# Kernel optimization log

Hardware: AMD Instinct MI355X
Metric: run time of the kernel (lower is better)

The kernel has to match this reference:

```python
import jax, jax.numpy as jnp
import numpy as np

DVEC = 128
B, S = 4, 1024


def setup_inputs() -> dict:
    key = jax.random.key(0)
    k1, k2 = jax.random.split(key)
    func_and_arg = jax.random.normal(k1, (B, S, 2 * DVEC), dtype=jnp.float32)
    cooccurrences = jax.random.normal(k2, (DVEC, DVEC, DVEC), dtype=jnp.float32)
    return {"func_and_arg": func_and_arg, "cooccurrences": cooccurrences}


def reference(func_and_arg, cooccurrences):
    # out[b,s,z] = sum_{i,j} func[b,s,i] * cooc[i,j,z] * arg[b,s,j]
    d = cooccurrences.shape[0]
    func = func_and_arg[..., :d]   # [B,S,D]
    arg = func_and_arg[..., d:]    # [B,S,D]
    # contract func over i first -> [B,S,D(j),Z], then arg over j -> [B,S,Z]
    tmp = jnp.einsum('bsi,ijz->bsjz', func, cooccurrences)
    return jnp.einsum('bsjz,bsj->bsz', tmp, arg)
```

## Files before the change

### kernel.cpp

```cpp
#include <hip/hip_runtime.h>
#include <hip/hip_bf16.h>


typedef __attribute__((ext_vector_type(8))) short bf16x8;
typedef __attribute__((ext_vector_type(4))) float f32x4;

__device__ __forceinline__ unsigned pkbf16(float x, float y) {
    __hip_bfloat162 h = __float22bfloat162_rn(make_float2(x, y));
    unsigned u; __builtin_memcpy(&u, &h, sizeof(u));
    return u;
}
__device__ __forceinline__ float bf16lo(unsigned u) {
    unsigned v = u << 16; float f; __builtin_memcpy(&f, &v, 4); return f;
}
__device__ __forceinline__ float bf16hi(unsigned u) {
    unsigned v = u & 0xFFFF0000u; float f; __builtin_memcpy(&f, &v, 4); return f;
}

__global__ __launch_bounds__(256) void cooc_prep(
    const float* __restrict__ Cc, const float* __restrict__ fa,
    ushort* __restrict__ CT, ushort* __restrict__ APK)
{
    const int bid = blockIdx.x;
    const int t = threadIdx.x;
    if (bid < 512) {
        __shared__ float tile[32][132];
        const int i  = bid >> 2;
        const int j0 = (bid & 3) * 32;
        {
            const int jj = t >> 3;
            const int zb = (t & 7) * 16;
            const float* src = Cc + (size_t)i * 16384 + (size_t)(j0 + jj) * 128 + zb;
            #pragma unroll
            for (int k = 0; k < 4; ++k)
                *(float4*)&tile[jj][zb + k * 4] = *(const float4*)(src + k * 4);
        }
        __syncthreads();
        {
            const int z = t >> 1;
            const int h = t & 1;
            unsigned o[8];
            #pragma unroll
            for (int p = 0; p < 8; ++p)
                o[p] = pkbf16(tile[h * 16 + 2 * p][z], tile[h * 16 + 2 * p + 1][z]);
            const int c0 = (j0 >> 3) + h * 2;
            ushort* dst = CT + (size_t)i * 16384 + (size_t)(z >> 4) * 2048
                             + (size_t)c0 * 128 + (z & 15) * 8;
            *(uint4*)dst         = make_uint4(o[0], o[1], o[2], o[3]);
            *(uint4*)(dst + 128) = make_uint4(o[4], o[5], o[6], o[7]);
        }
    } else {
        const int g = bid - 512;
        const int ks = t >> 6, lk = (t >> 4) & 3, lm = t & 15;
        (void)ks; (void)lk; (void)lm;
        const float* src = fa + (size_t)(g * 16 + (t & 15)) * 256 + 128
                              + (t >> 6) * 32 + ((t >> 4) & 3) * 8;
        float4 q0 = *(const float4*)src;
        float4 q1 = *(const float4*)(src + 4);
        *(uint4*)(APK + (size_t)g * 2048 + t * 8) =
            make_uint4(pkbf16(q0.x, q0.y), pkbf16(q0.z, q0.w),
                       pkbf16(q1.x, q1.y), pkbf16(q1.z, q1.w));
    }
}

template<int USE_WS>
__global__ __launch_bounds__(256, 3) void cooc_main(
    const float* __restrict__ fa, const ushort* __restrict__ CT,
    const ushort* __restrict__ APK, float* __restrict__ dst)
{
    __shared__ ushort fpk[16][128];

    const int bid = blockIdx.x;
    const int kp = bid & 7, zp = (bid >> 3) & 3, mtile = bid >> 5;
    const int t0 = mtile * 128, i0 = kp * 16;
    const int tid = threadIdx.x, lane = tid & 63, wv = tid >> 6;
    const int mg = wv >> 1, zg = wv & 1;
    const int lm = lane & 15, lk = lane >> 4;

    {
        const int row = tid & 127;
        const int sh = (tid >> 7) * 8;
        const float* fp = fa + (size_t)(t0 + row) * 256 + i0 + sh;
        float4 v0 = *(const float4*)fp;
        float4 v1 = *(const float4*)(fp + 4);
        fpk[sh + 0][row] = (ushort)(pkbf16(v0.x, v0.x) & 0xFFFF);
        fpk[sh + 1][row] = (ushort)(pkbf16(v0.y, v0.y) & 0xFFFF);
        fpk[sh + 2][row] = (ushort)(pkbf16(v0.z, v0.z) & 0xFFFF);
        fpk[sh + 3][row] = (ushort)(pkbf16(v0.w, v0.w) & 0xFFFF);
        fpk[sh + 4][row] = (ushort)(pkbf16(v1.x, v1.x) & 0xFFFF);
        fpk[sh + 5][row] = (ushort)(pkbf16(v1.y, v1.y) & 0xFFFF);
        fpk[sh + 6][row] = (ushort)(pkbf16(v1.z, v1.z) & 0xFFFF);
        fpk[sh + 7][row] = (ushort)(pkbf16(v1.w, v1.w) & 0xFFFF);
    }

    bf16x8 a_pk[4][4];
    {
        const ushort* ap = APK + (size_t)((t0 >> 4) + mg * 4) * 2048 + lane * 8;
        #pragma unroll
        for (int m = 0; m < 4; ++m)
            #pragma unroll
            for (int ks = 0; ks < 4; ++ks)
                a_pk[m][ks] = *(const bf16x8*)(ap + (size_t)m * 2048 + ks * 512);
    }

    const ushort* bbase = CT + (size_t)i0 * 16384
                             + (size_t)(zp * 2 + zg) * 2048 + lane * 8;

    bf16x8 Bg[2][4];
    #pragma unroll
    for (int c = 0; c < 4; ++c)
        Bg[0][c] = *(const bf16x8*)(bbase + c * 512);

    __syncthreads();

    float acc[4][4];
    #pragma unroll
    for (int m = 0; m < 4; ++m)
        #pragma unroll
        for (int r = 0; r < 4; ++r) acc[m][r] = 0.f;

    #pragma unroll 2
    for (int s = 0; s < 16; ++s) {
        const int cur = s & 1;

        if (s < 15) {
            const ushort* p = bbase + (size_t)(s + 1) * 16384;
            #pragma unroll
            for (int c = 0; c < 4; ++c)
                Bg[cur ^ 1][c] = *(const bf16x8*)(p + c * 512);
        }

        uint2 fq[4];
        #pragma unroll
        for (int m = 0; m < 4; ++m)
            fq[m] = *(const uint2*)&fpk[s][mg * 64 + m * 16 + lk * 4];

        f32x4 g[4];
        #pragma unroll
        for (int m = 0; m < 4; ++m) g[m] = (f32x4){0.f, 0.f, 0.f, 0.f};
        #pragma unroll
        for (int ks = 0; ks < 4; ++ks)
            #pragma unroll
            for (int m = 0; m < 4; ++m)
                g[m] = __builtin_amdgcn_mfma_f32_16x16x32_bf16(
                    a_pk[m][ks], Bg[cur][ks], g[m], 0, 0, 0);

        #pragma unroll
        for (int m = 0; m < 4; ++m) {
            acc[m][0] += bf16lo(fq[m].x) * g[m][0];
            acc[m][1] += bf16hi(fq[m].x) * g[m][1];
            acc[m][2] += bf16lo(fq[m].y) * g[m][2];
            acc[m][3] += bf16hi(fq[m].y) * g[m][3];
        }
    }

    const int col = zp * 32 + zg * 16 + lm;
    #pragma unroll
    for (int m = 0; m < 4; ++m)
        #pragma unroll
        for (int r = 0; r < 4; ++r) {
            const int row = t0 + mg * 64 + m * 16 + lk * 4 + r;
            if (USE_WS)
                dst[(size_t)kp * 524288 + (size_t)row * 128 + col] = acc[m][r];
            else
                atomicAdd(&dst[(size_t)row * 128 + col], acc[m][r]);
        }
}

__global__ __launch_bounds__(256) void cooc_reduce(const float* __restrict__ ws,
                                                   float* __restrict__ out) {
    const size_t idx = ((size_t)blockIdx.x * 256 + threadIdx.x) * 4;
    float4 a = *(const float4*)(ws + idx);
    #pragma unroll
    for (int k = 1; k < 8; ++k) {
        float4 b = *(const float4*)(ws + (size_t)k * 524288 + idx);
        a.x += b.x; a.y += b.y; a.z += b.z; a.w += b.w;
    }
    *(float4*)(out + idx) = a;
}

extern "C" void kernel_launch(void* const* d_in, const int* in_sizes, int n_in,
                              void* d_out, int out_size, void* d_ws, size_t ws_size,
                              hipStream_t stream) {
    const float* fa = (const float*)d_in[0];
    const float* Cc = (const float*)d_in[1];
    float* out = (float*)d_out;

    const size_t PART = (size_t)8 * 524288;
    const size_t CTOF = PART * sizeof(float);
    const size_t CTSZ = (size_t)128 * 128 * 128 * 2;
    const size_t APOF = CTOF + CTSZ;
    const size_t APSZ = (size_t)4096 * 128 * 2;
    const size_t NEED_FULL = APOF + APSZ;
    const size_t NEED_CT   = CTSZ + APSZ;

    if (ws_size >= NEED_FULL) {
        ushort* CT  = (ushort*)((char*)d_ws + CTOF);
        ushort* APK = (ushort*)((char*)d_ws + APOF);
        cooc_prep<<<768, 256, 0, stream>>>(Cc, fa, CT, APK);
        cooc_main<1><<<1024, 256, 0, stream>>>(fa, CT, APK, (float*)d_ws);
        cooc_reduce<<<512, 256, 0, stream>>>((const float*)d_ws, out);
    } else if (ws_size >= NEED_CT) {
        ushort* CT  = (ushort*)d_ws;
        ushort* APK = (ushort*)((char*)d_ws + CTSZ);
        cooc_prep<<<768, 256, 0, stream>>>(Cc, fa, CT, APK);
        (void)hipMemsetAsync(out, 0, (size_t)out_size * sizeof(float), stream);
        cooc_main<0><<<1024, 256, 0, stream>>>(fa, CT, APK, out);
    } else {
        (void)hipMemsetAsync(out, 0, (size_t)out_size * sizeof(float), stream);
        cooc_main<0><<<1024, 256, 0, stream>>>(fa, (const ushort*)d_ws,
                                               (const ushort*)d_ws, out);
    }
}
```

Before: 85.48 us.

## Double z-columns per wave to reuse A fragments, keep func in fp32 LDS

Each wave now computes two 16-wide z tiles instead of one. The A fragments held in registers and the func values in shared memory are reused across both tiles, and the grid is halved from 1024 to 512 blocks. Func values are stored as fp32 in shared memory, which removes the bf16 pack/unpack and uses the unrounded scale. This raises register pressure, so the occupancy hint drops to 2 blocks per CU, and having fewer blocks may lower latency hiding.

Result: no change. 84.63 us (-1.0%).

```diff
diff --git a/kernel.cpp b/kernel.cpp
--- a/kernel.cpp
+++ b/kernel.cpp
@@ -9,12 +9,6 @@
     __hip_bfloat162 h = __float22bfloat162_rn(make_float2(x, y));
     unsigned u; __builtin_memcpy(&u, &h, sizeof(u));
     return u;
-}
-__device__ __forceinline__ float bf16lo(unsigned u) {
-    unsigned v = u << 16; float f; __builtin_memcpy(&f, &v, 4); return f;
-}
-__device__ __forceinline__ float bf16hi(unsigned u) {
-    unsigned v = u & 0xFFFF0000u; float f; __builtin_memcpy(&f, &v, 4); return f;
 }
 
 __global__ __launch_bounds__(256) void cooc_prep(
@@ -51,8 +45,6 @@
         }
     } else {
         const int g = bid - 512;
-        const int ks = t >> 6, lk = (t >> 4) & 3, lm = t & 15;
-        (void)ks; (void)lk; (void)lm;
         const float* src = fa + (size_t)(g * 16 + (t & 15)) * 256 + 128
                               + (t >> 6) * 32 + ((t >> 4) & 3) * 8;
         float4 q0 = *(const float4*)src;
@@ -64,14 +56,14 @@
 }
 
 template<int USE_WS>
-__global__ __launch_bounds__(256, 3) void cooc_main(
+__global__ __launch_bounds__(256, 2) void cooc_main(
     const float* __restrict__ fa, const ushort* __restrict__ CT,
     const ushort* __restrict__ APK, float* __restrict__ dst)
 {
-    __shared__ ushort fpk[16][128];
+    __shared__ float fsh[16][128];
 
     const int bid = blockIdx.x;
-    const int kp = bid & 7, zp = (bid >> 3) & 3, mtile = bid >> 5;
+    const int kp = bid & 7, zh = (bid >> 3) & 1, mtile = bid >> 4;
     const int t0 = mtile * 128, i0 = kp * 16;
     const int tid = threadIdx.x, lane = tid & 63, wv = tid >> 6;
     const int mg = wv >> 1, zg = wv & 1;
@@ -83,14 +75,10 @@
         const float* fp = fa + (size_t)(t0 + row) * 256 + i0 + sh;
         float4 v0 = *(const float4*)fp;
         float4 v1 = *(const float4*)(fp + 4);
-        fpk[sh + 0][row] = (ushort)(pkbf16(v0.x, v0.x) & 0xFFFF);
-        fpk[sh + 1][row] = (ushort)(pkbf16(v0.y, v0.y) & 0xFFFF);
-        fpk[sh + 2][row] = (ushort)(pkbf16(v0.z, v0.z) & 0xFFFF);
-        fpk[sh + 3][row] = (ushort)(pkbf16(v0.w, v0.w) & 0xFFFF);
-        fpk[sh + 4][row] = (ushort)(pkbf16(v1.x, v1.x) & 0xFFFF);
-        fpk[sh + 5][row] = (ushort)(pkbf16(v1.y, v1.y) & 0xFFFF);
-        fpk[sh + 6][row] = (ushort)(pkbf16(v1.z, v1.z) & 0xFFFF);
-        fpk[sh + 7][row] = (ushort)(pkbf16(v1.w, v1.w) & 0xFFFF);
+        fsh[sh + 0][row] = v0.x; fsh[sh + 1][row] = v0.y;
+        fsh[sh + 2][row] = v0.z; fsh[sh + 3][row] = v0.w;
+        fsh[sh + 4][row] = v1.x; fsh[sh + 5][row] = v1.y;
+        fsh[sh + 6][row] = v1.z; fsh[sh + 7][row] = v1.w;
     }
 
     bf16x8 a_pk[4][4];
@@ -104,20 +92,24 @@
     }
 
     const ushort* bbase = CT + (size_t)i0 * 16384
-                             + (size_t)(zp * 2 + zg) * 2048 + lane * 8;
-
-    bf16x8 Bg[2][4];
-    #pragma unroll
-    for (int c = 0; c < 4; ++c)
-        Bg[0][c] = *(const bf16x8*)(bbase + c * 512);
+                             + (size_t)(zh * 4 + zg * 2) * 2048 + lane * 8;
+
+    bf16x8 Bg[2][2][4];
+    #pragma unroll
+    for (int zf = 0; zf < 2; ++zf)
+        #pragma unroll
+        for (int c = 0; c < 4; ++c)
+            Bg[0][zf][c] = *(const bf16x8*)(bbase + zf * 2048 + c * 512);
 
     __syncthreads();
 
-    float acc[4][4];
+    float acc[4][2][4];
     #pragma unroll
     for (int m = 0; m < 4; ++m)
         #pragma unroll
-        for (int r = 0; r < 4; ++r) acc[m][r] = 0.f;
+        for (int zf = 0; zf < 2; ++zf)
+            #pragma unroll
+            for (int r = 0; r < 4; ++r) acc[m][zf][r] = 0.f;
 
     #pragma unroll 2
     for (int s = 0; s < 16; ++s) {
@@ -126,45 +118,56 @@
         if (s < 15) {
             const ushort* p = bbase + (size_t)(s + 1) * 16384;
             #pragma unroll
-            for (int c = 0; c < 4; ++c)
-                Bg[cur ^ 1][c] = *(const bf16x8*)(p + c * 512);
+            for (int zf = 0; zf < 2; ++zf)
+                #pragma unroll
+                for (int c = 0; c < 4; ++c)
+                    Bg[cur ^ 1][zf][c] = *(const bf16x8*)(p + zf * 2048 + c * 512);
         }
 
-        uint2 fq[4];
-        #pragma unroll
-        for (int m = 0; m < 4; ++m)
-            fq[m] = *(const uint2*)&fpk[s][mg * 64 + m * 16 + lk * 4];
-
-        f32x4 g[4];
-        #pragma unroll
-        for (int m = 0; m < 4; ++m) g[m] = (f32x4){0.f, 0.f, 0.f, 0.f};
+        float4 fq[4];
+        #pragma unroll
+        for (int m = 0; m < 4; ++m)
+            fq[m] = *(const float4*)&fsh[s][mg * 64 + m * 16 + lk * 4];
+
+        f32x4 g[4][2];
+        #pragma unroll
+        for (int m = 0; m < 4; ++m)
+            #pragma unroll
+            for (int zf = 0; zf < 2; ++zf) g[m][zf] = (f32x4){0.f, 0.f, 0.f, 0.f};
         #pragma unroll
         for (int ks = 0; ks < 4; ++ks)
             #pragma unroll
             for (int m = 0; m < 4; ++m)
-                g[m] = __builtin_amdgcn_mfma_f32_16x16x32_bf16(
-                    a_pk[m][ks], Bg[cur][ks], g[m], 0, 0, 0);
-
-        #pragma unroll
-        for (int m = 0; m < 4; ++m) {
-            acc[m][0] += bf16lo(fq[m].x) * g[m][0];
-            acc[m][1] += bf16hi(fq[m].x) * g[m][1];
-            acc[m][2] += bf16lo(fq[m].y) * g[m][2];
-            acc[m][3] += bf16hi(fq[m].y) * g[m][3];
-        }
-    }
-
-    const int col = zp * 32 + zg * 16 + lm;
+                #pragma unroll
+                for (int zf = 0; zf < 2; ++zf)
+                    g[m][zf] = __builtin_amdgcn_mfma_f32_16x16x32_bf16(
+                        a_pk[m][ks], Bg[cur][zf][ks], g[m][zf], 0, 0, 0);
+
+        #pragma unroll
+        for (int m = 0; m < 4; ++m)
+            #pragma unroll
+            for (int zf = 0; zf < 2; ++zf) {
+                acc[m][zf][0] += fq[m].x * g[m][zf][0];
+                acc[m][zf][1] += fq[m].y * g[m][zf][1];
+                acc[m][zf][2] += fq[m].z * g[m][zf][2];
+                acc[m][zf][3] += fq[m].w * g[m][zf][3];
+            }
+    }
+
+    const int colbase = (zh * 4 + zg * 2) * 16 + lm;
     #pragma unroll
     for (int m = 0; m < 4; ++m)
         #pragma unroll
-        for (int r = 0; r < 4; ++r) {
-            const int row = t0 + mg * 64 + m * 16 + lk * 4 + r;
-            if (USE_WS)
-                dst[(size_t)kp * 524288 + (size_t)row * 128 + col] = acc[m][r];
-            else
-                atomicAdd(&dst[(size_t)row * 128 + col], acc[m][r]);
-        }
+        for (int zf = 0; zf < 2; ++zf)
+            #pragma unroll
+            for (int r = 0; r < 4; ++r) {
+                const int row = t0 + mg * 64 + m * 16 + lk * 4 + r;
+                const int col = colbase + zf * 16;
+                if (USE_WS)
+                    dst[(size_t)kp * 524288 + (size_t)row * 128 + col] = acc[m][zf][r];
+                else
+                    atomicAdd(&dst[(size_t)row * 128 + col], acc[m][zf][r]);
+            }
 }
 
 __global__ __launch_bounds__(256) void cooc_reduce(const float* __restrict__ ws,
@@ -198,17 +201,17 @@
         ushort* CT  = (ushort*)((char*)d_ws + CTOF);
         ushort* APK = (ushort*)((char*)d_ws + APOF);
         cooc_prep<<<768, 256, 0, stream>>>(Cc, fa, CT, APK);
-        cooc_main<1><<<1024, 256, 0, stream>>>(fa, CT, APK, (float*)d_ws);
+        cooc_main<1><<<512, 256, 0, stream>>>(fa, CT, APK, (float*)d_ws);
         cooc_reduce<<<512, 256, 0, stream>>>((const float*)d_ws, out);
     } else if (ws_size >= NEED_CT) {
         ushort* CT  = (ushort*)d_ws;
         ushort* APK = (ushort*)((char*)d_ws + CTSZ);
         cooc_prep<<<768, 256, 0, stream>>>(Cc, fa, CT, APK);
         (void)hipMemsetAsync(out, 0, (size_t)out_size * sizeof(float), stream);
-        cooc_main<0><<<1024, 256, 0, stream>>>(fa, CT, APK, out);
+        cooc_main<0><<<512, 256, 0, stream>>>(fa, CT, APK, out);
     } else {
         (void)hipMemsetAsync(out, 0, (size_t)out_size * sizeof(float), stream);
-        cooc_main<0><<<1024, 256, 0, stream>>>(fa, (const ushort*)d_ws,
-                                               (const ushort*)d_ws, out);
-    }
-}
+        cooc_main<0><<<512, 256, 0, stream>>>(fa, (const ushort*)d_ws,
+                                              (const ushort*)d_ws, out);
+    }
+}
```
